# Kernel tuning notes

Hardware: AMD Instinct MI355X
Metric: run time of the kernel (lower is better)

## Reference

```python
import jax, jax.numpy as jnp
import numpy as np

B, T, N, IN = 32, 12, 5000, 2
H, HOR, K, E = 128, 12, 3, 80000
NT = B * N  # total flattened nodes per timestep


def setup_inputs() -> dict:
    key = jax.random.key(0)
    ks = jax.random.split(key, 12)
    s = 0.05
    x = jax.random.normal(ks[0], (B, T, N, IN), jnp.float32)
    edge_index = jax.random.randint(ks[1], (2, E), 0, N, dtype=jnp.int64)
    W1 = jax.random.normal(ks[2], (K, IN, H), jnp.float32) * s
    b1 = jnp.zeros((H,), jnp.float32)
    W2 = jax.random.normal(ks[3], (K, H, H), jnp.float32) * s
    b2 = jnp.zeros((H,), jnp.float32)
    Wz = jax.random.normal(ks[4], (2 * H, H), jnp.float32) * s
    bz = jnp.zeros((H,), jnp.float32)
    Wr = jax.random.normal(ks[5], (2 * H, H), jnp.float32) * s
    br = jnp.zeros((H,), jnp.float32)
    Wc = jax.random.normal(ks[6], (2 * H, H), jnp.float32) * s
    bc = jnp.zeros((H,), jnp.float32)
    Wo = jax.random.normal(ks[7], (H, HOR), jnp.float32) * s  # output_dim=1 -> HOR*1
    bo = jnp.zeros((HOR,), jnp.float32)
    return dict(x=x, edge_index=edge_index, W1=W1, b1=b1, W2=W2, b2=b2,
                Wz=Wz, bz=bz, Wr=Wr, br=br, Wc=Wc, bc=bc, Wo=Wo, bo=bo)


def _cheb_norm(src, dst, num_total):
    # PyG sym-normalized Laplacian, lambda_max=2 -> L_hat = -D^-1/2 A D^-1/2, zero diag
    deg = jnp.zeros((num_total,), jnp.float32).at[src].add(1.0)
    dis = jnp.where(deg > 0, jax.lax.rsqrt(jnp.maximum(deg, 1.0)), 0.0)
    return -dis[src] * dis[dst]


def _cheb_conv(x, src, dst, norm, W, b):
    # x: [NT, F]; Chebyshev recursion T0=x, T1=L_hat x, Tk = 2 L_hat T_{k-1} - T_{k-2}
    def prop(t):
        return jnp.zeros_like(t).at[dst].add(norm[:, None] * t[src])
    Tx0 = x
    out = Tx0 @ W[0]
    Tx1 = prop(Tx0)
    out = out + Tx1 @ W[1]
    for k in range(2, W.shape[0]):
        Tx2 = 2.0 * prop(Tx1) - Tx0
        out = out + Tx2 @ W[k]
        Tx0, Tx1 = Tx1, Tx2
    return out + b


def reference(x, edge_index, W1, b1, W2, b2, Wz, bz, Wr, br, Wc, bc, Wo, bo):
    src, dst = edge_index[0], edge_index[1]
    norm = _cheb_norm(src, dst, NT)
    xt = jnp.transpose(x, (1, 0, 2, 3)).reshape(T, NT, IN)  # [T, B*N, IN]

    def step(h, x_t):
        ic = _cheb_conv(x_t, src, dst, norm, W1, b1)   # [NT, H]
        hc = _cheb_conv(h, src, dst, norm, W2, b2)     # [NT, H]
        comb = jnp.concatenate([ic, hc], axis=1)
        z = jax.nn.sigmoid(comb @ Wz + bz)
        r = jax.nn.sigmoid(comb @ Wr + br)
        h_tilde = jnp.tanh(jnp.concatenate([ic, r * hc], axis=1) @ Wc + bc)
        h_new = z * h + (1.0 - z) * h_tilde
        return h_new, None

    h0 = jnp.zeros((NT, H), jnp.float32)
    h, _ = jax.lax.scan(step, h0, xt)
    out = h @ Wo + bo                                  # [NT, HOR]
    out = out.reshape(B, N, HOR, 1)
    out = jnp.transpose(out, (0, 2, 1, 3)).squeeze(-1)  # [B, HOR, N]
    return out
```

## Files before the change

kernel.cpp:

```cpp
#include <hip/hip_runtime.h>
#include <hip/hip_bf16.h>

#define Bb  32
#define Tt  12
#define Nn  5000
#define INc 2
#define Hh  128
#define HORc 12
#define Ee  80000
#define NTt (Bb*Nn)

typedef float f4  __attribute__((ext_vector_type(4)));
typedef _Float16 h8 __attribute__((ext_vector_type(8)));
typedef _Float16 h4 __attribute__((ext_vector_type(4)));
typedef _Float16 h2 __attribute__((ext_vector_type(2)));

#define HSTRIDE 172
#define WAVE_LDS (32*HSTRIDE)

__device__ __forceinline__ float ldf(const void* p, size_t i, int isbf){
  return isbf ? __bfloat162float(((const __hip_bfloat16*)p)[i]) : ((const float*)p)[i];
}
__device__ __forceinline__ int eidx(const int* e, int i, int is64){
  return is64 ? e[2*i] : e[i];
}
__device__ __forceinline__ float sigm1(float x){
  return __builtin_amdgcn_rcpf(1.f + __expf(-x));
}
__device__ __forceinline__ float tanh1(float x){
  return 1.f - 2.f*__builtin_amdgcn_rcpf(1.f + __expf(2.f*x));
}

__global__ __launch_bounds__(256) void k_detect(const void* W2raw, const int* edge32, int* flags){
  __shared__ int cnt_bf, cnt_odd;
  if (threadIdx.x==0){ cnt_bf=0; cnt_odd=0; }
  __syncthreads();
  {
    unsigned w = ((const unsigned*)W2raw)[threadIdx.x];
    unsigned hb = (w>>8)&0x7Fu;
    if (hb>=0x34u && hb<=0x3Fu) atomicAdd(&cnt_bf,1);
  }
  if (threadIdx.x < 128){
    if (edge32[2*threadIdx.x+1] != 0) atomicAdd(&cnt_odd,1);
  }
  __syncthreads();
  if (threadIdx.x==0){
    flags[0] = (cnt_bf >= 128) ? 1 : 0;
    flags[1] = (cnt_odd == 0) ? 1 : 0;
  }
}

__global__ __launch_bounds__(256) void k_deg_cnt(const int* __restrict__ edge, int* deg, int* cnt,
                                                 const int* __restrict__ flags){
  int id = blockIdx.x*256 + threadIdx.x;
  int is64 = flags[1];
  if (id < Ee){
    atomicAdd(&deg[eidx(edge, id, is64)], 1);
    atomicAdd(&cnt[eidx(edge, Ee+id, is64)], 1);
  }
}

__global__ __launch_bounds__(256) void k_dis(const int* __restrict__ deg, float* dis){
  int id = blockIdx.x*256 + threadIdx.x;
  if (id < Nn){
    int d = deg[id];
    dis[id] = d > 0 ? rsqrtf((float)d) : 0.f;
  }
}

__global__ __launch_bounds__(1024) void k_scan(const int* __restrict__ cnt, int* rowptr){
  __shared__ int part[1024];
  int t = threadIdx.x;
  int base = t*5;
  int s = 0;
  #pragma unroll
  for (int j=0;j<5;j++){ int idx=base+j; if (idx<Nn) s += cnt[idx]; }
  part[t] = s; __syncthreads();
  for (int off=1; off<1024; off<<=1){
    int add = (t>=off) ? part[t-off] : 0;
    __syncthreads();
    part[t] += add;
    __syncthreads();
  }
  int run = (t>0) ? part[t-1] : 0;
  #pragma unroll
  for (int j=0;j<5;j++){
    int idx = base+j;
    if (idx < Nn){ rowptr[idx] = run; run += cnt[idx]; }
  }
  if (t == 1023) rowptr[Nn] = part[1023];
}

__global__ __launch_bounds__(256) void k_fill(const int* __restrict__ edge,
                                              const int* __restrict__ rowptr,
                                              int* fillc, int* csr,
                                              const int* __restrict__ flags){
  int id = blockIdx.x*256 + threadIdx.x;
  int is64 = flags[1];
  if (id < Ee){
    int d = eidx(edge, Ee+id, is64);
    int pos = atomicAdd(&fillc[d], 1);
    csr[rowptr[d] + pos] = eidx(edge, id, is64);
  }
}

__global__ __launch_bounds__(128) void k_wx(
  const void* __restrict__ W1, const void* __restrict__ b1,
  const void* __restrict__ W2, const void* __restrict__ b2,
  const void* __restrict__ Wz, const void* __restrict__ bz,
  const void* __restrict__ Wr, const void* __restrict__ br,
  const void* __restrict__ Wc, const void* __restrict__ bc,
  _Float16* __restrict__ Wext, _Float16* __restrict__ Whc,
  const int* __restrict__ flags)
{
  int bid = blockIdx.x, f = threadIdx.x;
  int isbf = flags[0];
  if (bid < 640){
    int s = bid/160, k = bid - s*160;
    float v = 0.f;
    if (k < 128){
      if (s == 0)
        v = ldf(W2,(size_t)k*128+f,isbf) - ldf(W2,(size_t)(2*128+k)*128+f,isbf);
      else {
        const void* Wg = (s==1)?Wz:((s==2)?Wr:Wc);
        v = ldf(Wg,(size_t)(128+k)*128+f,isbf);
      }
    } else if (s == 0){
      v = (k==128) ? ldf(b2,f,isbf) : 0.f;
    } else if (k < 134){
      const void* Wg = (s==1)?Wz:((s==2)?Wr:Wc);
      int q = k - 128;
      float acc = 0.f;
      for (int j=0;j<128;j++) acc += ldf(W1,(size_t)q*128+j,isbf)*ldf(Wg,(size_t)j*128+f,isbf);
      v = acc;
    } else if (k == 134){
      const void* Wg = (s==1)?Wz:((s==2)?Wr:Wc);
      const void* bg = (s==1)?bz:((s==2)?br:bc);
      float acc = ldf(bg,f,isbf);
      for (int j=0;j<128;j++) acc += ldf(b1,j,isbf)*ldf(Wg,(size_t)j*128+f,isbf);
      v = acc;
    }
    Wext[(size_t)(s*128+f)*160 + k] = (_Float16)v;
  } else {
    int k = bid - 640;
    float v = (k < 128) ? ldf(W2,(size_t)(128+k)*128+f,isbf)
                        : 2.f*ldf(W2,(size_t)(2*128+(k-128))*128+f,isbf);
    Whc[(size_t)f*256 + k] = (_Float16)v;
  }
}

__global__ __launch_bounds__(256) void k_px1(
  const void* __restrict__ x, const float* __restrict__ dis,
  const int* __restrict__ rowptr, const int* __restrict__ csr, float* __restrict__ px1,
  const int* __restrict__ flags)
{
  int id = blockIdx.x*256 + threadIdx.x;
  int isbf = flags[0];
  if (id < Tt*Nn){
    int t = id / Nn, n = id - t*Nn;
    int e0 = rowptr[n], e1 = rowptr[n+1];
    float a0=0.f, a1=0.f;
    for (int e=e0;e<e1;e++){
      int s = csr[e]; float ds = dis[s];
      size_t xb = (size_t)(t*Nn+s)*2;
      a0 += ds*ldf(x,xb+0,isbf); a1 += ds*ldf(x,xb+1,isbf);
    }
    float dn = -dis[n];
    px1[id*2+0] = dn*a0; px1[id*2+1] = dn*a1;
  }
}

__global__ __launch_bounds__(256) void k_px2(
  const float* __restrict__ px1, const float* __restrict__ dis,
  const int* __restrict__ rowptr, const int* __restrict__ csr, float* __restrict__ px2)
{
  int id = blockIdx.x*256 + threadIdx.x;
  if (id < Tt*Nn){
    int t = id / Nn, n = id - t*Nn;
    int e0 = rowptr[n], e1 = rowptr[n+1];
    float a0=0.f, a1=0.f;
    for (int e=e0;e<e1;e++){
      int s = csr[e]; float ds = dis[s];
      const float* pp = px1 + (size_t)(t*Nn+s)*2;
      a0 += ds*pp[0]; a1 += ds*pp[1];
    }
    float dn = -dis[n];
    px2[id*2+0] = dn*a0; px2[id*2+1] = dn*a1;
  }
}

__global__ __launch_bounds__(256) void k_ph1(
  const _Float16* __restrict__ h16, const float* __restrict__ dis,
  const int* __restrict__ rowptr, const int* __restrict__ csr,
  _Float16* __restrict__ phh)
{
  int n = blockIdx.x*4 + (threadIdx.x>>6);
  int f2 = threadIdx.x & 63;
  int e0 = rowptr[n], e1 = rowptr[n+1];
  float a0=0.f, a1=0.f, b0=0.f, b1=0.f;
  int e = e0;
  for (; e+3 < e1; e += 4){
    int s0=csr[e], s1=csr[e+1], s2=csr[e+2], s3=csr[e+3];
    float d0=dis[s0], d1=dis[s1], d2=dis[s2], d3=dis[s3];
    h2 v0 = *(const h2*)(h16 + (size_t)s0*128 + 2*f2);
    h2 v1 = *(const h2*)(h16 + (size_t)s1*128 + 2*f2);
    h2 v2 = *(const h2*)(h16 + (size_t)s2*128 + 2*f2);
    h2 v3 = *(const h2*)(h16 + (size_t)s3*128 + 2*f2);
    a0 += d0*(float)v0[0]; a1 += d0*(float)v0[1];
    b0 += d1*(float)v1[0]; b1 += d1*(float)v1[1];
    a0 += d2*(float)v2[0]; a1 += d2*(float)v2[1];
    b0 += d3*(float)v3[0]; b1 += d3*(float)v3[1];
  }
  for (; e < e1; e++){
    int s = csr[e]; float ds = dis[s];
    h2 v = *(const h2*)(h16 + (size_t)s*128 + 2*f2);
    a0 += ds*(float)v[0]; a1 += ds*(float)v[1];
  }
  a0 += b0; a1 += b1;
  float dn = -dis[n];
  h2 o; o[0]=(_Float16)(dn*a0); o[1]=(_Float16)(dn*a1);
  *(h2*)(phh + (size_t)n*256 + 2*f2) = o;
}

__global__ __launch_bounds__(256) void k_ph2(
  const float* __restrict__ dis,
  const int* __restrict__ rowptr, const int* __restrict__ csr,
  _Float16* __restrict__ phh)
{
  int n = blockIdx.x*4 + (threadIdx.x>>6);
  int f2 = threadIdx.x & 63;
  int e0 = rowptr[n], e1 = rowptr[n+1];
  float a0=0.f, a1=0.f, b0=0.f, b1=0.f;
  int e = e0;
  for (; e+3 < e1; e += 4){
    int s0=csr[e], s1=csr[e+1], s2=csr[e+2], s3=csr[e+3];
    float d0=dis[s0], d1=dis[s1], d2=dis[s2], d3=dis[s3];
    h2 v0 = *(const h2*)(phh + (size_t)s0*256 + 2*f2);
    h2 v1 = *(const h2*)(phh + (size_t)s1*256 + 2*f2);
    h2 v2 = *(const h2*)(phh + (size_t)s2*256 + 2*f2);
    h2 v3 = *(const h2*)(phh + (size_t)s3*256 + 2*f2);
    a0 += d0*(float)v0[0]; a1 += d0*(float)v0[1];
    b0 += d1*(float)v1[0]; b1 += d1*(float)v1[1];
    a0 += d2*(float)v2[0]; a1 += d2*(float)v2[1];
    b0 += d3*(float)v3[0]; b1 += d3*(float)v3[1];
  }
  for (; e < e1; e++){
    int s = csr[e]; float ds = dis[s];
    h2 v = *(const h2*)(phh + (size_t)s*256 + 2*f2);
    a0 += ds*(float)v[0]; a1 += ds*(float)v[1];
  }
  a0 += b0; a1 += b1;
  float dn = -dis[n];
  h2 o; o[0]=(_Float16)(dn*a0); o[1]=(_Float16)(dn*a1);
  *(h2*)(phh + (size_t)n*256 + 128 + 2*f2) = o;
}


__device__ __forceinline__ void load_b(const _Float16* hcL, h8 (&bf)[2][5], int lane){
  int n16 = lane & 15, q8 = (lane>>4)*8;
  #pragma unroll
  for (int tl=0;tl<2;tl++)
    #pragma unroll
    for (int ks=0;ks<5;ks++)
      bf[tl][ks] = *(const h8*)&hcL[(tl*16+n16)*HSTRIDE + ks*32 + q8];
}

__device__ __forceinline__ void st0(
  const _Float16* __restrict__ Wst, const _Float16* __restrict__ Whc,
  const _Float16* __restrict__ h16, const _Float16* __restrict__ phh,
  _Float16* __restrict__ hcL, int gbase, int lane)
{
  int n16 = lane & 15, g = lane >> 4, q8 = g*8;
  h8 zz = {0,0,0,0,0,0,0,0};
  h8 bf[2][5];
  #pragma unroll
  for (int tl=0;tl<2;tl++){
    const _Float16* hp = h16 + (size_t)(gbase + tl*16 + n16)*128 + q8;
    #pragma unroll
    for (int ks=0;ks<4;ks++) bf[tl][ks] = *(const h8*)(hp + ks*32);
    h8 e = zz;
    if (g==0) e[0] = (_Float16)1.f;
    bf[tl][4] = e;
  }
  bool graph = (gbase < Nn);
  h8 bg[2][8];
  if (graph){
    #pragma unroll
    for (int tl=0;tl<2;tl++){
      int node = gbase + tl*16 + n16;
      int row = node < Nn ? node : 0;
      bool ok = node < Nn;
      const _Float16* pp = phh + (size_t)row*256 + q8;
      #pragma unroll
      for (int ks=0;ks<8;ks++){
        h8 v = *(const h8*)(pp + ks*32);
        bg[tl][ks] = ok ? v : zz;
      }
    }
  }
  f4 z4 = {0.f,0.f,0.f,0.f};
  #pragma unroll
  for (int fp=0; fp<4; fp++){
    f4 acc[2][2];
    #pragma unroll
    for (int tl=0;tl<2;tl++){ acc[tl][0]=z4; acc[tl][1]=z4; }
    const _Float16* Wa = Wst + (size_t)(fp*32 + n16)*160 + q8;
    #pragma unroll
    for (int ks=0; ks<5; ks++){
      h8 a0 = *(const h8*)(Wa + ks*32);
      h8 a1 = *(const h8*)(Wa + 16*160 + ks*32);
      #pragma unroll
      for (int tl=0;tl<2;tl++){
        acc[tl][0] = __builtin_amdgcn_mfma_f32_16x16x32_f16(a0, bf[tl][ks], acc[tl][0], 0,0,0);
        acc[tl][1] = __builtin_amdgcn_mfma_f32_16x16x32_f16(a1, bf[tl][ks], acc[tl][1], 0,0,0);
      }
    }
    if (graph){
      const _Float16* Wb = Whc + (size_t)(fp*32 + n16)*256 + q8;
      #pragma unroll
      for (int ks=0; ks<8; ks++){
        h8 a0 = *(const h8*)(Wb + ks*32);
        h8 a1 = *(const h8*)(Wb + 16*256 + ks*32);
        #pragma unroll
        for (int tl=0;tl<2;tl++){
          acc[tl][0] = __builtin_amdgcn_mfma_f32_16x16x32_f16(a0, bg[tl][ks], acc[tl][0], 0,0,0);
          acc[tl][1] = __builtin_amdgcn_mfma_f32_16x16x32_f16(a1, bg[tl][ks], acc[tl][1], 0,0,0);
        }
      }
    }
    #pragma unroll
    for (int tl=0;tl<2;tl++)
      #pragma unroll
      for (int hh=0;hh<2;hh++){
        int fb = fp*32 + hh*16 + g*4;
        f4 a = acc[tl][hh];
        h4 o;
        #pragma unroll
        for (int r=0;r<4;r++) o[r] = (_Float16)a[r];
        *(h4*)&hcL[(tl*16+n16)*HSTRIDE + fb] = o;
      }
  }
}

template<int S>
__device__ __forceinline__ void mm_stage(
  const _Float16* __restrict__ Wst, const h8 (&bf)[2][5],
  _Float16* __restrict__ hcL, h4 (&zr)[4][2][2],
  _Float16* __restrict__ h16, int gbase, int lane)
{
  int n16 = lane & 15, g = lane >> 4, q8 = g*8;
  f4 z4 = {0.f,0.f,0.f,0.f};
  #pragma unroll
  for (int fp=0; fp<4; fp++){
    f4 acc[2][2];
    #pragma unroll
    for (int tl=0;tl<2;tl++){ acc[tl][0]=z4; acc[tl][1]=z4; }
    const _Float16* Wa = Wst + (size_t)(fp*32 + n16)*160 + q8;
    #pragma unroll
    for (int ks=0; ks<5; ks++){
      h8 a0 = *(const h8*)(Wa + ks*32);
      h8 a1 = *(const h8*)(Wa + 16*160 + ks*32);
      #pragma unroll
      for (int tl=0;tl<2;tl++){
        acc[tl][0] = __builtin_amdgcn_mfma_f32_16x16x32_f16(a0, bf[tl][ks], acc[tl][0], 0,0,0);
        acc[tl][1] = __builtin_amdgcn_mfma_f32_16x16x32_f16(a1, bf[tl][ks], acc[tl][1], 0,0,0);
      }
    }
    #pragma unroll
    for (int tl=0;tl<2;tl++)
      #pragma unroll
      for (int hh=0;hh<2;hh++){
        int fb = fp*32 + hh*16 + g*4;
        int nn = tl*16 + n16;
        f4 a = acc[tl][hh];
        if (S == 1){
          h4 o;
          #pragma unroll
          for (int r=0;r<4;r++) o[r] = (_Float16)sigm1(a[r]);
          zr[fp][tl][hh] = o;
        } else if (S == 2){
          h4 hcv = *(const h4*)&hcL[nn*HSTRIDE + fb];
          h4 o;
          #pragma unroll
          for (int r=0;r<4;r++) o[r] = (_Float16)(sigm1(a[r]) * (float)hcv[r]);
          *(h4*)&hcL[nn*HSTRIDE + fb] = o;
        } else {
          int gi = gbase + nn;
          h4 ho = *(const h4*)(h16 + (size_t)gi*128 + fb);
          h4 zv = zr[fp][tl][hh];
          h4 o;
          #pragma unroll
          for (int r=0;r<4;r++){
            float z = (float)zv[r];
            o[r] = (_Float16)(z*(float)ho[r] + (1.f - z)*tanh1(a[r]));
          }
          *(h4*)(h16 + (size_t)gi*128 + fb) = o;
        }
      }
  }
}

__global__ __launch_bounds__(256, 2) void k_mainm(
    _Float16* __restrict__ h16, const void* __restrict__ x,
    const float* __restrict__ px1, const float* __restrict__ px2,
    const _Float16* __restrict__ phh,
    const _Float16* __restrict__ Wext, const _Float16* __restrict__ Whc,
    const int* __restrict__ flags, int t)
{
  __shared__ _Float16 smem[4*WAVE_LDS];
  int tid = threadIdx.x;
  int w = tid >> 6, lane = tid & 63;
  int gbase = blockIdx.x*128 + w*32;
  _Float16* hcL = smem + w*WAVE_LDS;

  if (lane < 32){
    int n = lane;
    _Float16* row = hcL + n*HSTRIDE;
    for (int k=135;k<160;k++) row[k] = (_Float16)0.f;
    int isbf = flags[0];
    int i = gbase + n;
    int b = i / Nn, nn2 = i - b*Nn;
    size_t xb = ((size_t)(b*Tt + t)*Nn + nn2)*2;
    float x0 = ldf(x,xb+0,isbf), x1 = ldf(x,xb+1,isbf);
    float u1a=0.f,u1b=0.f,u2a=-x0,u2b=-x1;
    if (i < Nn){
      u1a = px1[(t*Nn+i)*2+0]; u1b = px1[(t*Nn+i)*2+1];
      u2a = 2.f*px2[(t*Nn+i)*2+0] - x0; u2b = 2.f*px2[(t*Nn+i)*2+1] - x1;
    }
    row[128]=(_Float16)x0;  row[129]=(_Float16)x1;
    row[130]=(_Float16)u1a; row[131]=(_Float16)u1b;
    row[132]=(_Float16)u2a; row[133]=(_Float16)u2b;
    row[134]=(_Float16)1.f;
  }

  st0(Wext, Whc, h16, phh, hcL, gbase, lane);

  h4 zr[4][2][2];

  h8 ba[2][5];
  load_b(hcL, ba, lane);
  mm_stage<1>(Wext + 1*20480, ba, hcL, zr, h16, gbase, lane);
  mm_stage<2>(Wext + 2*20480, ba, hcL, zr, h16, gbase, lane);

  h8 bc[2][5];
  load_b(hcL, bc, lane);
  mm_stage<3>(Wext + 3*20480, bc, hcL, zr, h16, gbase, lane);
}

__global__ __launch_bounds__(256) void k_out(
  const _Float16* __restrict__ h16, const void* __restrict__ Wo,
  const void* __restrict__ bo, void* __restrict__ out,
  const int* __restrict__ flags)
{
  __shared__ float wol[128*HORc];
  __shared__ float wob[HORc];
  int isbf = flags[0];
  for (int idx=threadIdx.x; idx<128*HORc; idx+=256) wol[idx] = ldf(Wo, idx, isbf);
  if (threadIdx.x < HORc) wob[threadIdx.x] = ldf(bo, threadIdx.x, isbf);
  __syncthreads();

  int i = blockIdx.x*256 + threadIdx.x;
  if (i < NTt){
    float acc[HORc];
    #pragma unroll
    for (int j=0;j<HORc;j++) acc[j] = wob[j];
    const _Float16* hp = h16 + (size_t)i*128;
    for (int kb=0;kb<16;kb++){
      h8 hv = *(const h8*)(hp + kb*8);
      #pragma unroll
      for (int j=0;j<8;j++){
        float hvf = (float)hv[j];
        #pragma unroll
        for (int jj=0;jj<HORc;jj++) acc[jj] += hvf * wol[(kb*8+j)*HORc + jj];
      }
    }
    int b = i / Nn, n = i - b*Nn;
    #pragma unroll
    for (int j=0;j<HORc;j++){
      size_t oi = (size_t)(b*HORc+j)*Nn + n;
      if (isbf) ((__hip_bfloat16*)out)[oi] = __float2bfloat16(acc[j]);
      else      ((float*)out)[oi] = acc[j];
    }
  }
}

extern "C" void kernel_launch(void* const* d_in, const int* in_sizes, int n_in,
                              void* d_out, int out_size, void* d_ws, size_t ws_size,
                              hipStream_t stream) {
  (void)in_sizes; (void)n_in; (void)out_size; (void)ws_size;
  const void* x   = d_in[0];
  const int*  edge= (const int*)d_in[1];
  const void* W1  = d_in[2];
  const void* b1  = d_in[3];
  const void* W2  = d_in[4];
  const void* b2  = d_in[5];
  const void* Wz  = d_in[6];
  const void* bz  = d_in[7];
  const void* Wr  = d_in[8];
  const void* br  = d_in[9];
  const void* Wc  = d_in[10];
  const void* bc  = d_in[11];
  const void* Wo  = d_in[12];
  const void* bo  = d_in[13];

  char* ws = (char*)d_ws;
  size_t off = 0;
  auto alloc = [&](size_t bytes)->char*{
    char* p = ws + off;
    off += (bytes + 255) & ~(size_t)255;
    return p;
  };
  _Float16* h16  = (_Float16*)alloc((size_t)NTt*128*2);
  int*   deg   = (int*)  alloc(Nn*4);
  int*   cnt   = (int*)  alloc(Nn*4);
  int*   fillc = (int*)  alloc(Nn*4);
  size_t zlen = off;
  int*   flags = (int*)  alloc(16*4);
  float* dis   = (float*)alloc(Nn*4);
  int*   rowptr= (int*)  alloc((Nn+1)*4);
  int*   csr   = (int*)  alloc(Ee*4);
  float* px1   = (float*)alloc((size_t)Tt*Nn*2*4);
  float* px2   = (float*)alloc((size_t)Tt*Nn*2*4);
  _Float16* phh  = (_Float16*)alloc((size_t)5120*256*2);
  _Float16* Wext = (_Float16*)alloc((size_t)4*128*160*2);
  _Float16* Whc  = (_Float16*)alloc((size_t)128*256*2);

  hipMemsetAsync(d_ws, 0, zlen, stream);

  k_detect <<<1,256,0,stream>>>(W2, edge, flags);
  k_deg_cnt<<<(Ee+255)/256,256,0,stream>>>(edge, deg, cnt, flags);
  k_dis    <<<(Nn+255)/256,256,0,stream>>>(deg, dis);
  k_scan   <<<1,1024,0,stream>>>(cnt, rowptr);
  k_fill   <<<(Ee+255)/256,256,0,stream>>>(edge, rowptr, fillc, csr, flags);
  k_wx     <<<896,128,0,stream>>>(W1,b1,W2,b2,Wz,bz,Wr,br,Wc,bc, Wext, Whc, flags);
  k_px1    <<<(Tt*Nn+255)/256,256,0,stream>>>(x, dis, rowptr, csr, px1, flags);
  k_px2    <<<(Tt*Nn+255)/256,256,0,stream>>>(px1, dis, rowptr, csr, px2);

  for (int t=0; t<Tt; ++t){
    k_ph1  <<<Nn/4,256,0,stream>>>(h16, dis, rowptr, csr, phh);
    k_ph2  <<<Nn/4,256,0,stream>>>(dis, rowptr, csr, phh);
    k_mainm<<<NTt/128,256,0,stream>>>(h16, x, px1, px2, phh, Wext, Whc, flags, t);
  }

  k_out<<<(NTt+255)/256,256,0,stream>>>(h16, Wo, bo, d_out, flags);
}
```

Baseline: 1.373 ms.

## Split output features across waves sharing a 64-node LDS tile in GRU kernel

```diff
diff --git a/kernel.cpp b/kernel.cpp
--- a/kernel.cpp
+++ b/kernel.cpp
@@ -16,7 +16,7 @@
 typedef _Float16 h2 __attribute__((ext_vector_type(2)));
 
 #define HSTRIDE 172
-#define WAVE_LDS (32*HSTRIDE)
+#define GROUP_LDS (64*HSTRIDE)
 
 __device__ __forceinline__ float ldf(const void* p, size_t i, int isbf){
   return isbf ? __bfloat162float(((const __hip_bfloat16*)p)[i]) : ((const float*)p)[i];
@@ -256,150 +256,6 @@
 }
 
 
-__device__ __forceinline__ void load_b(const _Float16* hcL, h8 (&bf)[2][5], int lane){
-  int n16 = lane & 15, q8 = (lane>>4)*8;
-  #pragma unroll
-  for (int tl=0;tl<2;tl++)
-    #pragma unroll
-    for (int ks=0;ks<5;ks++)
-      bf[tl][ks] = *(const h8*)&hcL[(tl*16+n16)*HSTRIDE + ks*32 + q8];
-}
-
-__device__ __forceinline__ void st0(
-  const _Float16* __restrict__ Wst, const _Float16* __restrict__ Whc,
-  const _Float16* __restrict__ h16, const _Float16* __restrict__ phh,
-  _Float16* __restrict__ hcL, int gbase, int lane)
-{
-  int n16 = lane & 15, g = lane >> 4, q8 = g*8;
-  h8 zz = {0,0,0,0,0,0,0,0};
-  h8 bf[2][5];
-  #pragma unroll
-  for (int tl=0;tl<2;tl++){
-    const _Float16* hp = h16 + (size_t)(gbase + tl*16 + n16)*128 + q8;
-    #pragma unroll
-    for (int ks=0;ks<4;ks++) bf[tl][ks] = *(const h8*)(hp + ks*32);
-    h8 e = zz;
-    if (g==0) e[0] = (_Float16)1.f;
-    bf[tl][4] = e;
-  }
-  bool graph = (gbase < Nn);
-  h8 bg[2][8];
-  if (graph){
-    #pragma unroll
-    for (int tl=0;tl<2;tl++){
-      int node = gbase + tl*16 + n16;
-      int row = node < Nn ? node : 0;
-      bool ok = node < Nn;
-      const _Float16* pp = phh + (size_t)row*256 + q8;
-      #pragma unroll
-      for (int ks=0;ks<8;ks++){
-        h8 v = *(const h8*)(pp + ks*32);
-        bg[tl][ks] = ok ? v : zz;
-      }
-    }
-  }
-  f4 z4 = {0.f,0.f,0.f,0.f};
-  #pragma unroll
-  for (int fp=0; fp<4; fp++){
-    f4 acc[2][2];
-    #pragma unroll
-    for (int tl=0;tl<2;tl++){ acc[tl][0]=z4; acc[tl][1]=z4; }
-    const _Float16* Wa = Wst + (size_t)(fp*32 + n16)*160 + q8;
-    #pragma unroll
-    for (int ks=0; ks<5; ks++){
-      h8 a0 = *(const h8*)(Wa + ks*32);
-      h8 a1 = *(const h8*)(Wa + 16*160 + ks*32);
-      #pragma unroll
-      for (int tl=0;tl<2;tl++){
-        acc[tl][0] = __builtin_amdgcn_mfma_f32_16x16x32_f16(a0, bf[tl][ks], acc[tl][0], 0,0,0);
-        acc[tl][1] = __builtin_amdgcn_mfma_f32_16x16x32_f16(a1, bf[tl][ks], acc[tl][1], 0,0,0);
-      }
-    }
-    if (graph){
-      const _Float16* Wb = Whc + (size_t)(fp*32 + n16)*256 + q8;
-      #pragma unroll
-      for (int ks=0; ks<8; ks++){
-        h8 a0 = *(const h8*)(Wb + ks*32);
-        h8 a1 = *(const h8*)(Wb + 16*256 + ks*32);
-        #pragma unroll
-        for (int tl=0;tl<2;tl++){
-          acc[tl][0] = __builtin_amdgcn_mfma_f32_16x16x32_f16(a0, bg[tl][ks], acc[tl][0], 0,0,0);
-          acc[tl][1] = __builtin_amdgcn_mfma_f32_16x16x32_f16(a1, bg[tl][ks], acc[tl][1], 0,0,0);
-        }
-      }
-    }
-    #pragma unroll
-    for (int tl=0;tl<2;tl++)
-      #pragma unroll
-      for (int hh=0;hh<2;hh++){
-        int fb = fp*32 + hh*16 + g*4;
-        f4 a = acc[tl][hh];
-        h4 o;
-        #pragma unroll
-        for (int r=0;r<4;r++) o[r] = (_Float16)a[r];
-        *(h4*)&hcL[(tl*16+n16)*HSTRIDE + fb] = o;
-      }
-  }
-}
-
-template<int S>
-__device__ __forceinline__ void mm_stage(
-  const _Float16* __restrict__ Wst, const h8 (&bf)[2][5],
-  _Float16* __restrict__ hcL, h4 (&zr)[4][2][2],
-  _Float16* __restrict__ h16, int gbase, int lane)
-{
-  int n16 = lane & 15, g = lane >> 4, q8 = g*8;
-  f4 z4 = {0.f,0.f,0.f,0.f};
-  #pragma unroll
-  for (int fp=0; fp<4; fp++){
-    f4 acc[2][2];
-    #pragma unroll
-    for (int tl=0;tl<2;tl++){ acc[tl][0]=z4; acc[tl][1]=z4; }
-    const _Float16* Wa = Wst + (size_t)(fp*32 + n16)*160 + q8;
-    #pragma unroll
-    for (int ks=0; ks<5; ks++){
-      h8 a0 = *(const h8*)(Wa + ks*32);
-      h8 a1 = *(const h8*)(Wa + 16*160 + ks*32);
-      #pragma unroll
-      for (int tl=0;tl<2;tl++){
-        acc[tl][0] = __builtin_amdgcn_mfma_f32_16x16x32_f16(a0, bf[tl][ks], acc[tl][0], 0,0,0);
-        acc[tl][1] = __builtin_amdgcn_mfma_f32_16x16x32_f16(a1, bf[tl][ks], acc[tl][1], 0,0,0);
-      }
-    }
-    #pragma unroll
-    for (int tl=0;tl<2;tl++)
-      #pragma unroll
-      for (int hh=0;hh<2;hh++){
-        int fb = fp*32 + hh*16 + g*4;
-        int nn = tl*16 + n16;
-        f4 a = acc[tl][hh];
-        if (S == 1){
-          h4 o;
-          #pragma unroll
-          for (int r=0;r<4;r++) o[r] = (_Float16)sigm1(a[r]);
-          zr[fp][tl][hh] = o;
-        } else if (S == 2){
-          h4 hcv = *(const h4*)&hcL[nn*HSTRIDE + fb];
-          h4 o;
-          #pragma unroll
-          for (int r=0;r<4;r++) o[r] = (_Float16)(sigm1(a[r]) * (float)hcv[r]);
-          *(h4*)&hcL[nn*HSTRIDE + fb] = o;
-        } else {
-          int gi = gbase + nn;
-          h4 ho = *(const h4*)(h16 + (size_t)gi*128 + fb);
-          h4 zv = zr[fp][tl][hh];
-          h4 o;
-          #pragma unroll
-          for (int r=0;r<4;r++){
-            float z = (float)zv[r];
-            o[r] = (_Float16)(z*(float)ho[r] + (1.f - z)*tanh1(a[r]));
-          }
-          *(h4*)(h16 + (size_t)gi*128 + fb) = o;
-        }
-      }
-  }
-}
-
 __global__ __launch_bounds__(256, 2) void k_mainm(
     _Float16* __restrict__ h16, const void* __restrict__ x,
     const float* __restrict__ px1, const float* __restrict__ px2,
@@ -407,14 +263,15 @@
     const _Float16* __restrict__ Wext, const _Float16* __restrict__ Whc,
     const int* __restrict__ flags, int t)
 {
-  __shared__ _Float16 smem[4*WAVE_LDS];
+  __shared__ _Float16 hcL[GROUP_LDS];
   int tid = threadIdx.x;
   int w = tid >> 6, lane = tid & 63;
-  int gbase = blockIdx.x*128 + w*32;
-  _Float16* hcL = smem + w*WAVE_LDS;
-
-  if (lane < 32){
-    int n = lane;
+  int fp = w;
+  int gbase = blockIdx.x*64;
+  int n16 = lane & 15, g = lane >> 4, q8 = g*8;
+
+  if (tid < 64){
+    int n = tid;
     _Float16* row = hcL + n*HSTRIDE;
     for (int k=135;k<160;k++) row[k] = (_Float16)0.f;
     int isbf = flags[0];
@@ -433,18 +290,185 @@
     row[134]=(_Float16)1.f;
   }
 
-  st0(Wext, Whc, h16, phh, hcL, gbase, lane);
-
-  h4 zr[4][2][2];
-
-  h8 ba[2][5];
-  load_b(hcL, ba, lane);
-  mm_stage<1>(Wext + 1*20480, ba, hcL, zr, h16, gbase, lane);
-  mm_stage<2>(Wext + 2*20480, ba, hcL, zr, h16, gbase, lane);
-
-  h8 bc[2][5];
-  load_b(hcL, bc, lane);
-  mm_stage<3>(Wext + 3*20480, bc, hcL, zr, h16, gbase, lane);
+  h8 zz = {0,0,0,0,0,0,0,0};
+  h8 biasv = zz;
+  if (g==0) biasv[0] = (_Float16)1.f;
+  f4 z4 = {0.f,0.f,0.f,0.f};
+
+  f4 acc[4][2];
+  #pragma unroll
+  for (int tl=0;tl<4;tl++){ acc[tl][0]=z4; acc[tl][1]=z4; }
+  {
+    h8 bf[4][4];
+    #pragma unroll
+    for (int tl=0;tl<4;tl++){
+      const _Float16* hp = h16 + (size_t)(gbase + tl*16 + n16)*128 + q8;
+      #pragma unroll
+      for (int ks=0;ks<4;ks++) bf[tl][ks] = *(const h8*)(hp + ks*32);
+    }
+    const _Float16* Wa = Wext + (size_t)(fp*32 + n16)*160 + q8;
+    #pragma unroll
+    for (int ks=0; ks<5; ks++){
+      h8 a0 = *(const h8*)(Wa + ks*32);
+      h8 a1 = *(const h8*)(Wa + 16*160 + ks*32);
+      #pragma unroll
+      for (int tl=0;tl<4;tl++){
+        h8 b = (ks<4) ? bf[tl][ks] : biasv;
+        acc[tl][0] = __builtin_amdgcn_mfma_f32_16x16x32_f16(a0, b, acc[tl][0], 0,0,0);
+        acc[tl][1] = __builtin_amdgcn_mfma_f32_16x16x32_f16(a1, b, acc[tl][1], 0,0,0);
+      }
+    }
+  }
+  if (gbase < Nn){
+    const _Float16* Wb = Whc + (size_t)(fp*32 + n16)*256 + q8;
+    #pragma unroll
+    for (int pass=0; pass<2; pass++){
+      h8 bg[2][8];
+      #pragma unroll
+      for (int tt=0;tt<2;tt++){
+        int node = gbase + (pass*2+tt)*16 + n16;
+        bool ok = node < Nn;
+        const _Float16* pp = phh + (size_t)(ok ? node : 0)*256 + q8;
+        #pragma unroll
+        for (int ks=0;ks<8;ks++){
+          h8 v = *(const h8*)(pp + ks*32);
+          bg[tt][ks] = ok ? v : zz;
+        }
+      }
+      #pragma unroll
+      for (int ks=0; ks<8; ks++){
+        h8 a0 = *(const h8*)(Wb + ks*32);
+        h8 a1 = *(const h8*)(Wb + 16*256 + ks*32);
+        #pragma unroll
+        for (int tt=0;tt<2;tt++){
+          acc[pass*2+tt][0] = __builtin_amdgcn_mfma_f32_16x16x32_f16(a0, bg[tt][ks], acc[pass*2+tt][0], 0,0,0);
+          acc[pass*2+tt][1] = __builtin_amdgcn_mfma_f32_16x16x32_f16(a1, bg[tt][ks], acc[pass*2+tt][1], 0,0,0);
+        }
+      }
+    }
+  }
+  #pragma unroll
+  for (int tl=0;tl<4;tl++)
+    #pragma unroll
+    for (int hh=0;hh<2;hh++){
+      int fb = fp*32 + hh*16 + g*4;
+      f4 a = acc[tl][hh];
+      h4 o;
+      #pragma unroll
+      for (int r=0;r<4;r++) o[r] = (_Float16)a[r];
+      *(h4*)&hcL[(tl*16+n16)*HSTRIDE + fb] = o;
+    }
+
+  __syncthreads();
+
+  h8 ba[4][5];
+  #pragma unroll
+  for (int tl=0;tl<4;tl++)
+    #pragma unroll
+    for (int ks=0;ks<5;ks++)
+      ba[tl][ks] = *(const h8*)&hcL[(tl*16+n16)*HSTRIDE + ks*32 + q8];
+
+  f4 accZ[4][2];
+  #pragma unroll
+  for (int tl=0;tl<4;tl++){ accZ[tl][0]=z4; accZ[tl][1]=z4; }
+  {
+    const _Float16* Wa = Wext + 1*20480 + (size_t)(fp*32 + n16)*160 + q8;
+    #pragma unroll
+    for (int ks=0; ks<5; ks++){
+      h8 a0 = *(const h8*)(Wa + ks*32);
+      h8 a1 = *(const h8*)(Wa + 16*160 + ks*32);
+      #pragma unroll
+      for (int tl=0;tl<4;tl++){
+        accZ[tl][0] = __builtin_amdgcn_mfma_f32_16x16x32_f16(a0, ba[tl][ks], accZ[tl][0], 0,0,0);
+        accZ[tl][1] = __builtin_amdgcn_mfma_f32_16x16x32_f16(a1, ba[tl][ks], accZ[tl][1], 0,0,0);
+      }
+    }
+  }
+  h4 zr[4][2];
+  #pragma unroll
+  for (int tl=0;tl<4;tl++)
+    #pragma unroll
+    for (int hh=0;hh<2;hh++){
+      f4 a = accZ[tl][hh];
+      h4 o;
+      #pragma unroll
+      for (int r=0;r<4;r++) o[r] = (_Float16)sigm1(a[r]);
+      zr[tl][hh] = o;
+    }
+
+  f4 accR[4][2];
+  #pragma unroll
+  for (int tl=0;tl<4;tl++){ accR[tl][0]=z4; accR[tl][1]=z4; }
+  {
+    const _Float16* Wa = Wext + 2*20480 + (size_t)(fp*32 + n16)*160 + q8;
+    #pragma unroll
+    for (int ks=0; ks<5; ks++){
+      h8 a0 = *(const h8*)(Wa + ks*32);
+      h8 a1 = *(const h8*)(Wa + 16*160 + ks*32);
+      #pragma unroll
+      for (int tl=0;tl<4;tl++){
+        accR[tl][0] = __builtin_amdgcn_mfma_f32_16x16x32_f16(a0, ba[tl][ks], accR[tl][0], 0,0,0);
+        accR[tl][1] = __builtin_amdgcn_mfma_f32_16x16x32_f16(a1, ba[tl][ks], accR[tl][1], 0,0,0);
+      }
+    }
+  }
+  #pragma unroll
+  for (int tl=0;tl<4;tl++)
+    #pragma unroll
+    for (int hh=0;hh<2;hh++){
+      int fb = fp*32 + hh*16 + g*4;
+      int nn = tl*16 + n16;
+      h4 hcv = *(const h4*)&hcL[nn*HSTRIDE + fb];
+      f4 a = accR[tl][hh];
+      h4 o;
+      #pragma unroll
+      for (int r=0;r<4;r++) o[r] = (_Float16)(sigm1(a[r]) * (float)hcv[r]);
+      *(h4*)&hcL[nn*HSTRIDE + fb] = o;
+    }
+
+  __syncthreads();
+
+  h8 bc[4][5];
+  #pragma unroll
+  for (int tl=0;tl<4;tl++)
+    #pragma unroll
+    for (int ks=0;ks<5;ks++)
+      bc[tl][ks] = *(const h8*)&hcL[(tl*16+n16)*HSTRIDE + ks*32 + q8];
+
+  f4 accC[4][2];
+  #pragma unroll
+  for (int tl=0;tl<4;tl++){ accC[tl][0]=z4; accC[tl][1]=z4; }
+  {
+    const _Float16* Wa = Wext + 3*20480 + (size_t)(fp*32 + n16)*160 + q8;
+    #pragma unroll
+    for (int ks=0; ks<5; ks++){
+      h8 a0 = *(const h8*)(Wa + ks*32);
+      h8 a1 = *(const h8*)(Wa + 16*160 + ks*32);
+      #pragma unroll
+      for (int tl=0;tl<4;tl++){
+        accC[tl][0] = __builtin_amdgcn_mfma_f32_16x16x32_f16(a0, bc[tl][ks], accC[tl][0], 0,0,0);
+        accC[tl][1] = __builtin_amdgcn_mfma_f32_16x16x32_f16(a1, bc[tl][ks], accC[tl][1], 0,0,0);
+      }
+    }
+  }
+  #pragma unroll
+  for (int tl=0;tl<4;tl++)
+    #pragma unroll
+    for (int hh=0;hh<2;hh++){
+      int fb = fp*32 + hh*16 + g*4;
+      int nn = tl*16 + n16;
+      int gi = gbase + nn;
+      h4 ho = *(const h4*)(h16 + (size_t)gi*128 + fb);
+      h4 zv = zr[tl][hh];
+      f4 a = accC[tl][hh];
+      h4 o;
+      #pragma unroll
+      for (int r=0;r<4;r++){
+        float z = (float)zv[r];
+        o[r] = (_Float16)(z*(float)ho[r] + (1.f - z)*tanh1(a[r]));
+      }
+      *(h4*)(h16 + (size_t)gi*128 + fb) = o;
+    }
 }
 
 __global__ __launch_bounds__(256) void k_out(
@@ -539,7 +563,7 @@
   for (int t=0; t<Tt; ++t){
     k_ph1  <<<Nn/4,256,0,stream>>>(h16, dis, rowptr, csr, phh);
     k_ph2  <<<Nn/4,256,0,stream>>>(dis, rowptr, csr, phh);
-    k_mainm<<<NTt/128,256,0,stream>>>(h16, x, px1, px2, phh, Wext, Whc, flags, t);
+    k_mainm<<<NTt/64,256,0,stream>>>(h16, x, px1, px2, phh, Wext, Whc, flags, t);
   }
 
   k_out<<<(NTt+255)/256,256,0,stream>>>(h16, Wo, bo, d_out, flags);
```

After: 1.136 ms. 17.3% less time.
